# Performance work log

Hardware: AMD Instinct MI355X
Metric: run time of the kernel (lower is better)

The kernel has to match this reference:

```python
import jax, jax.numpy as jnp
import numpy as np

HEAD_DIM = 128
HIDDEN = 5120
NUM_KV_GROUPS = 8
NUM_MODALITIES = 3
NUM_Q_HEADS = 40
QKV_PER_MOD = NUM_Q_HEADS * HEAD_DIM + 2 * NUM_KV_GROUPS * HEAD_DIM + NUM_Q_HEADS  # 7208


def _rms_norm(x, w, eps=1e-6):
    xf = x.astype(jnp.float32)
    inv = jax.lax.rsqrt(jnp.mean(xf * xf, axis=-1, keepdims=True) + eps)
    return (xf * inv).astype(x.dtype) * w


def _apply_rope(x, cos, sin):
    # x: [B,S,H,D], cos/sin: [B,S,rd]
    rd = cos.shape[-1]
    xr, xp = x[..., :rd], x[..., rd:]
    c, s = cos[:, :, None, :], sin[:, :, None, :]
    x1, x2 = xr[..., : rd // 2], xr[..., rd // 2:]
    rot = jnp.concatenate([-x2, x1], axis=-1)
    return jnp.concatenate([xr * c + rot * s, xp], axis=-1)


def setup_inputs() -> dict:
    key = jax.random.key(0)
    ks = jax.random.split(key, 6)
    B, S = 1, 2048
    return {
        "x": jax.random.normal(ks[0], (B, S, HIDDEN), jnp.float32),
        "rope_cos": jax.random.uniform(ks[1], (B, S, HEAD_DIM), jnp.float32),
        "rope_sin": jax.random.uniform(ks[2], (B, S, HEAD_DIM), jnp.float32),
        "modality_ids": jax.random.randint(ks[3], (B, S), 0, NUM_MODALITIES, jnp.int32),
        "pre_norm": jnp.ones((NUM_MODALITIES * HIDDEN,), jnp.float32),
        "qkv_w": jax.random.normal(ks[4], (NUM_MODALITIES * QKV_PER_MOD, HIDDEN), jnp.float32) * 0.02,
        "q_norm": jnp.ones((NUM_MODALITIES * HEAD_DIM,), jnp.float32),
        "k_norm": jnp.ones((NUM_MODALITIES * HEAD_DIM,), jnp.float32),
        "proj_w": jax.random.normal(ks[5], (NUM_MODALITIES * HIDDEN, HIDDEN), jnp.float32) * 0.02,
    }


def reference(x, rope_cos, rope_sin, modality_ids, pre_norm, qkv_w, q_norm, k_norm, proj_w):
    B, S, _ = x.shape
    # per-token modality gather of pre-norm weight
    norm_w = pre_norm.reshape(NUM_MODALITIES, HIDDEN)[modality_ids]  # [B,S,H]
    normed = _rms_norm(x, norm_w)

    # modality-routed QKV: compute all modalities, select with one-hot (dense, jit-friendly)
    oh = jax.nn.one_hot(modality_ids, NUM_MODALITIES, dtype=x.dtype)  # [B,S,M]
    qkv_w3 = qkv_w.reshape(NUM_MODALITIES, QKV_PER_MOD, HIDDEN)
    qkv_all = jnp.einsum("bsh,moh->bsmo", normed, qkv_w3)  # [B,S,M,QKV]
    qkv = jnp.einsum("bsm,bsmo->bso", oh, qkv_all)

    q_dim = NUM_Q_HEADS * HEAD_DIM
    k_dim = NUM_KV_GROUPS * HEAD_DIM
    q = qkv[..., :q_dim].reshape(B, S, NUM_Q_HEADS, HEAD_DIM)
    k = qkv[..., q_dim:q_dim + k_dim].reshape(B, S, NUM_KV_GROUPS, HEAD_DIM)
    v = qkv[..., q_dim + k_dim:q_dim + 2 * k_dim].reshape(B, S, NUM_KV_GROUPS, HEAD_DIM)
    gate = jax.nn.sigmoid(qkv[..., q_dim + 2 * k_dim:q_dim + 2 * k_dim + NUM_Q_HEADS])  # [B,S,NQ]

    qn = q_norm.reshape(NUM_MODALITIES, HEAD_DIM)[modality_ids][:, :, None, :]  # [B,S,1,D]
    kn = k_norm.reshape(NUM_MODALITIES, HEAD_DIM)[modality_ids][:, :, None, :]
    q = _rms_norm(q, qn)
    k = _rms_norm(k, kn)

    q = _apply_rope(q, rope_cos, rope_sin)
    k = _apply_rope(k, rope_cos, rope_sin)

    repeat = NUM_Q_HEADS // NUM_KV_GROUPS
    k = jnp.repeat(k, repeat, axis=2)  # [B,S,NQ,D]
    v = jnp.repeat(v, repeat, axis=2)

    scale = 1.0 / np.sqrt(HEAD_DIM)
    scores = jnp.einsum("bqhd,bkhd->bhqk", q, k) * scale  # [B,NQ,S,S]
    attn = jax.nn.softmax(scores, axis=-1)
    out = jnp.einsum("bhqk,bkhd->bqhd", attn, v)  # [B,S,NQ,D]

    out = (out * gate[..., None]).reshape(B, S, NUM_Q_HEADS * HEAD_DIM)

    proj_w3 = proj_w.reshape(NUM_MODALITIES, HIDDEN, HIDDEN)
    proj_all = jnp.einsum("bsh,moh->bsmo", out, proj_w3)  # [B,S,M,H]
    return jnp.einsum("bsm,bsmo->bso", oh, proj_all)
```

## Files before the change

kernel.cpp:

```cpp
#include <hip/hip_runtime.h>

typedef _Float16 f16;
typedef f16 f16x8 __attribute__((ext_vector_type(8)));
typedef f16 f16x4 __attribute__((ext_vector_type(4)));
typedef float f32x4 __attribute__((ext_vector_type(4)));

#define HID 5120
#define QKVO 7208
#define S_TOK 2048
#define NQH 40
#define NKV 8
#define HD 128

__device__ __forceinline__ void gload16(const void* g, void* l) {
    __builtin_amdgcn_global_load_lds(
        (const __attribute__((address_space(1))) void*)g,
        (__attribute__((address_space(3))) void*)l,
        16, 0, 0);
}

__global__ void sort_tokens(const int* __restrict__ mod, int* __restrict__ sorted,
                            int* __restrict__ offs)
{
    int tid = threadIdx.x, wave = tid >> 6, lane = tid & 63;
    int mloc[8];
    int c[3] = {0, 0, 0};
#pragma unroll
    for (int j = 0; j < 8; ++j) {
        int m = mod[tid * 8 + j];
        mloc[j] = m;
        c[m]++;
    }
    __shared__ int wsum[4][3];
    int excl[3];
#pragma unroll
    for (int m = 0; m < 3; ++m) {
        int v = c[m];
        int incl = v;
        for (int d = 1; d < 64; d <<= 1) {
            int n = __shfl_up(incl, d, 64);
            if (lane >= d) incl += n;
        }
        excl[m] = incl - v;
        if (lane == 63) wsum[wave][m] = incl;
    }
    __syncthreads();
    int wbase[3], tot[3];
#pragma unroll
    for (int m = 0; m < 3; ++m) {
        int b = 0, t = 0;
        for (int w = 0; w < 4; ++w) {
            if (w < wave) b += wsum[w][m];
            t += wsum[w][m];
        }
        wbase[m] = b;
        tot[m] = t;
    }
    int base[3];
    base[0] = 0;
    base[1] = tot[0];
    base[2] = tot[0] + tot[1];
    if (tid == 0) {
        offs[0] = 0;
        offs[1] = tot[0];
        offs[2] = tot[0] + tot[1];
        offs[3] = S_TOK;
    }
    int pos[3];
#pragma unroll
    for (int m = 0; m < 3; ++m) pos[m] = base[m] + wbase[m] + excl[m];
#pragma unroll
    for (int j = 0; j < 8; ++j) {
        int m = mloc[j];
        sorted[pos[m]++] = tid * 8 + j;
    }
}

__global__ void cvt_f32_f16(const float* __restrict__ src, f16* __restrict__ dst, int n4)
{
    int i = blockIdx.x * 256 + threadIdx.x;
    int stride = gridDim.x * 256;
    const float4* s4 = (const float4*)src;
    f16x4* d4 = (f16x4*)dst;
    for (; i < n4; i += stride) {
        float4 a = s4[i];
        f16x4 h;
        h[0] = (f16)a.x; h[1] = (f16)a.y; h[2] = (f16)a.z; h[3] = (f16)a.w;
        d4[i] = h;
    }
}

__global__ void rms_pre(const float* __restrict__ x, const int* __restrict__ mod,
                        const float* __restrict__ prenorm, f16* __restrict__ A1)
{
    int tok = blockIdx.x, tid = threadIdx.x;
    int m = mod[tok];
    const float4* xv = (const float4*)(x + (size_t)tok * HID);
    float4 v[5];
    float ss = 0.f;
#pragma unroll
    for (int j = 0; j < 5; ++j) {
        v[j] = xv[tid + 256 * j];
        ss += v[j].x * v[j].x + v[j].y * v[j].y + v[j].z * v[j].z + v[j].w * v[j].w;
    }
    for (int d = 1; d < 64; d <<= 1) ss += __shfl_xor(ss, d, 64);
    __shared__ float ws[4];
    if ((tid & 63) == 0) ws[tid >> 6] = ss;
    __syncthreads();
    float tot = ws[0] + ws[1] + ws[2] + ws[3];
    float inv = rsqrtf(tot * (1.f / HID) + 1e-6f);
    const float4* wv = (const float4*)(prenorm + (size_t)m * HID);
    f16x4* out4 = (f16x4*)(A1 + (size_t)tok * HID);
#pragma unroll
    for (int j = 0; j < 5; ++j) {
        float4 w = wv[tid + 256 * j];
        f16x4 h;
        h[0] = (f16)(v[j].x * inv * w.x);
        h[1] = (f16)(v[j].y * inv * w.y);
        h[2] = (f16)(v[j].z * inv * w.z);
        h[3] = (f16)(v[j].w * inv * w.w);
        out4[tid + 256 * j] = h;
    }
}

__global__ void gemm_grouped(const f16* __restrict__ A, const f16* __restrict__ W,
                             float* __restrict__ C,
                             const int* __restrict__ sorted_tok,
                             const int* __restrict__ mod_off, int NW)
{
    const int K = HID;
    int nt = blockIdx.x, mt = blockIdx.y, mod = blockIdx.z;
    int off = mod_off[mod], cnt = mod_off[mod + 1] - off;
    if (mt * 128 >= cnt) return;
    __shared__ __align__(16) f16 As[128 * 64];
    __shared__ __align__(16) f16 Bs[128 * 64];
    __shared__ int rowtok[128];
    int tid = threadIdx.x, wave = tid >> 6, lane = tid & 63;
    if (tid < 128) {
        int r = mt * 128 + tid;
        rowtok[tid] = (r < cnt) ? sorted_tok[off + r] : -1;
    }
    __syncthreads();
    int wr = wave >> 1, wc = wave & 1;
    f32x4 acc[4][4] = {};
    const f16* Wm = W + (size_t)mod * NW * K;
    for (int kt = 0; kt < K / 64; ++kt) {
        int k0 = kt * 64;
#pragma unroll
        for (int it = 0; it < 4; ++it) {
            int c = it * 256 + tid;
            int row = c >> 3, kc = c & 7, skc = kc ^ (row & 7);
            int tk = rowtok[row];
            if (tk < 0) tk = 0;
            gload16(A + (size_t)tk * K + k0 + skc * 8, &As[c * 8]);
        }
#pragma unroll
        for (int it = 0; it < 4; ++it) {
            int c = it * 256 + tid;
            int row = c >> 3, kc = c & 7, skc = kc ^ (row & 7);
            int o = nt * 128 + row;
            if (o >= NW) o = NW - 1;
            gload16(Wm + (size_t)o * K + k0 + skc * 8, &Bs[c * 8]);
        }
        __syncthreads();
#pragma unroll
        for (int ks = 0; ks < 2; ++ks) {
            f16x8 a[4], b[4];
#pragma unroll
            for (int i = 0; i < 4; ++i) {
                int ar = wr * 64 + i * 16 + (lane & 15);
                int ac = (ks * 4 + (lane >> 4)) ^ (ar & 7);
                a[i] = *(const f16x8*)&As[ar * 64 + ac * 8];
                int br = wc * 64 + i * 16 + (lane & 15);
                int bc = (ks * 4 + (lane >> 4)) ^ (br & 7);
                b[i] = *(const f16x8*)&Bs[br * 64 + bc * 8];
            }
#pragma unroll
            for (int mi = 0; mi < 4; ++mi)
#pragma unroll
                for (int nj = 0; nj < 4; ++nj)
                    acc[mi][nj] = __builtin_amdgcn_mfma_f32_16x16x32_f16(
                        a[mi], b[nj], acc[mi][nj], 0, 0, 0);
        }
        __syncthreads();
    }
    int cl = lane & 15, rg = lane >> 4;
#pragma unroll
    for (int mi = 0; mi < 4; ++mi) {
#pragma unroll
        for (int rr = 0; rr < 4; ++rr) {
            int row = wr * 64 + mi * 16 + rg * 4 + rr;
            int tk = rowtok[row];
            if (tk < 0) continue;
            float* crow = C + (size_t)tk * NW;
#pragma unroll
            for (int nj = 0; nj < 4; ++nj) {
                int o = nt * 128 + wc * 64 + nj * 16 + cl;
                if (o < NW) crow[o] = acc[mi][nj][rr];
            }
        }
    }
}

__global__ void qkv_post(const float* __restrict__ qkv, const int* __restrict__ mod,
                         const float* __restrict__ cosb, const float* __restrict__ sinb,
                         const float* __restrict__ qnorm, const float* __restrict__ knorm,
                         f16* __restrict__ Qb, f16* __restrict__ Kb, float* __restrict__ gateb)
{
    int tok = blockIdx.x, tid = threadIdx.x;
    int wave = tid >> 6, lane = tid & 63;
    int m = mod[tok];
    float c0 = cosb[tok * HD + lane], c1 = cosb[tok * HD + 64 + lane];
    float s0 = sinb[tok * HD + lane], s1 = sinb[tok * HD + 64 + lane];
    const float* row = qkv + (size_t)tok * QKVO;
    for (int u = wave; u < 48; u += 4) {
        int base = (u < 40) ? u * HD : NQH * HD + (u - 40) * HD;
        float x0 = row[base + lane];
        float x1 = row[base + 64 + lane];
        float ss = x0 * x0 + x1 * x1;
        for (int d = 1; d < 64; d <<= 1) ss += __shfl_xor(ss, d, 64);
        float inv = rsqrtf(ss * (1.f / HD) + 1e-6f);
        const float* nw = (u < 40 ? qnorm : knorm) + m * HD;
        float n0 = x0 * inv * nw[lane];
        float n1 = x1 * inv * nw[64 + lane];
        float r0 = n0 * c0 - n1 * s0;
        float r1 = n1 * c1 + n0 * s1;
        if (u < 40) {
            const float sc = 0.08838834764831845f;
            r0 *= sc; r1 *= sc;
            Qb[((size_t)u * S_TOK + tok) * HD + lane] = (f16)r0;
            Qb[((size_t)u * S_TOK + tok) * HD + 64 + lane] = (f16)r1;
        } else {
            Kb[((size_t)(u - 40) * S_TOK + tok) * HD + lane] = (f16)r0;
            Kb[((size_t)(u - 40) * S_TOK + tok) * HD + 64 + lane] = (f16)r1;
        }
    }
    if (tid < 40) {
        float g = row[NQH * HD + 2 * NKV * HD + tid];
        gateb[tok * 40 + tid] = 1.f / (1.f + __expf(-g));
    }
}

__global__ void vtrans(const float* __restrict__ qkv, f16* __restrict__ Vt)
{
    int tc = blockIdx.x;
    int g = blockIdx.y;
    int tid = threadIdx.x;
    __shared__ float tile[64][129];
#pragma unroll
    for (int it = 0; it < 8; ++it) {
        int idx = it * 256 + tid;
        int r = idx >> 5, c4 = idx & 31;
        float4 v = *(const float4*)(qkv + (size_t)(tc * 64 + r) * QKVO + NQH * HD + NKV * HD + g * HD + c4 * 4);
        tile[r][c4 * 4 + 0] = v.x;
        tile[r][c4 * 4 + 1] = v.y;
        tile[r][c4 * 4 + 2] = v.z;
        tile[r][c4 * 4 + 3] = v.w;
    }
    __syncthreads();
    int d = tid >> 1, half = tid & 1;
    f16* dst = Vt + ((size_t)g * HD + d) * S_TOK + tc * 64 + half * 32;
#pragma unroll
    for (int j = 0; j < 32; ++j) dst[j] = (f16)tile[half * 32 + j][d];
}

__global__ void attn(const f16* __restrict__ Qb, const f16* __restrict__ Kb,
                     const f16* __restrict__ Vtb, const float* __restrict__ gateb,
                     f16* __restrict__ A2)
{
    int qt = blockIdx.x, h = blockIdx.y, grp = h / 5;
    int tid = threadIdx.x, wave = tid >> 6, lane = tid & 63;
    __shared__ __align__(16) f16 Qs[64 * 128];
    __shared__ __align__(16) f16 Ks[64 * 128];
    __shared__ __align__(16) f16 Vs[128 * 64];
    __shared__ __align__(16) f16 Ps[4][16 * 64];
    const f16* Qg = Qb + ((size_t)h * S_TOK + qt * 64) * HD;
#pragma unroll
    for (int it = 0; it < 4; ++it) {
        int c = it * 256 + tid, row = c >> 4, kc = c & 15, skc = kc ^ (row & 15);
        gload16(Qg + row * HD + skc * 8, &Qs[c * 8]);
    }
    __syncthreads();
    f16x8 qf[4];
    {
        int row = wave * 16 + (lane & 15);
#pragma unroll
        for (int ks = 0; ks < 4; ++ks) {
            int sk = (ks * 4 + (lane >> 4)) ^ (row & 15);
            qf[ks] = *(const f16x8*)&Qs[row * 128 + sk * 8];
        }
    }
    f32x4 o[8] = {};
    float mrow[4] = {-3.0e38f, -3.0e38f, -3.0e38f, -3.0e38f};
    float lrow[4] = {0.f, 0.f, 0.f, 0.f};
    const f16* Kg = Kb + (size_t)grp * S_TOK * HD;
    const f16* Vg = Vtb + (size_t)grp * HD * S_TOK;
    char* pbase = (char*)&Ps[wave][0];
    for (int t = 0; t < 32; ++t) {
#pragma unroll
        for (int it = 0; it < 4; ++it) {
            int c = it * 256 + tid, row = c >> 4, kc = c & 15, skc = kc ^ (row & 15);
            gload16(Kg + (size_t)(t * 64 + row) * HD + skc * 8, &Ks[c * 8]);
        }
#pragma unroll
        for (int it = 0; it < 4; ++it) {
            int c = it * 256 + tid, row = c >> 3, kc = c & 7, skc = kc ^ (row & 7);
            gload16(Vg + (size_t)row * S_TOK + t * 64 + skc * 8, &Vs[c * 8]);
        }
        __syncthreads();
        f32x4 s[4] = {};
#pragma unroll
        for (int ks = 0; ks < 4; ++ks) {
#pragma unroll
            for (int nj = 0; nj < 4; ++nj) {
                int kr = nj * 16 + (lane & 15);
                int sk = (ks * 4 + (lane >> 4)) ^ (kr & 15);
                f16x8 kf = *(const f16x8*)&Ks[kr * 128 + sk * 8];
                s[nj] = __builtin_amdgcn_mfma_f32_16x16x32_f16(qf[ks], kf, s[nj], 0, 0, 0);
            }
        }
        float mx[4], corr[4], psum[4];
#pragma unroll
        for (int r = 0; r < 4; ++r)
            mx[r] = fmaxf(fmaxf(s[0][r], s[1][r]), fmaxf(s[2][r], s[3][r]));
        for (int d = 1; d < 16; d <<= 1) {
#pragma unroll
            for (int r = 0; r < 4; ++r) mx[r] = fmaxf(mx[r], __shfl_xor(mx[r], d, 16));
        }
#pragma unroll
        for (int r = 0; r < 4; ++r) {
            float mn = fmaxf(mrow[r], mx[r]);
            corr[r] = __expf(mrow[r] - mn);
            mrow[r] = mn;
            psum[r] = 0.f;
        }
#pragma unroll
        for (int nj = 0; nj < 4; ++nj) {
#pragma unroll
            for (int r = 0; r < 4; ++r) {
                float p = __expf(s[nj][r] - mrow[r]);
                psum[r] += p;
                int prow = (lane >> 4) * 4 + r, col = (lane & 15) + nj * 16;
                int addr = (prow * 128 + col * 2) ^ ((prow & 7) << 4);
                *(f16*)(pbase + addr) = (f16)p;
            }
        }
        for (int d = 1; d < 16; d <<= 1) {
#pragma unroll
            for (int r = 0; r < 4; ++r) psum[r] += __shfl_xor(psum[r], d, 16);
        }
#pragma unroll
        for (int r = 0; r < 4; ++r) lrow[r] = lrow[r] * corr[r] + psum[r];
#pragma unroll
        for (int nj2 = 0; nj2 < 8; ++nj2)
#pragma unroll
            for (int r = 0; r < 4; ++r) o[nj2][r] *= corr[r];
#pragma unroll
        for (int ks2 = 0; ks2 < 2; ++ks2) {
            int prow = lane & 15;
            int sk = (ks2 * 4 + (lane >> 4)) ^ (prow & 7);
            f16x8 pa = *(const f16x8*)(pbase + prow * 128 + sk * 16);
#pragma unroll
            for (int nj2 = 0; nj2 < 8; ++nj2) {
                int vr = nj2 * 16 + (lane & 15);
                int skv = (ks2 * 4 + (lane >> 4)) ^ (vr & 7);
                f16x8 vf = *(const f16x8*)&Vs[vr * 64 + skv * 8];
                o[nj2] = __builtin_amdgcn_mfma_f32_16x16x32_f16(pa, vf, o[nj2], 0, 0, 0);
            }
        }
        __syncthreads();
    }
    int rbase = qt * 64 + wave * 16 + (lane >> 4) * 4;
#pragma unroll
    for (int r = 0; r < 4; ++r) {
        int tok = rbase + r;
        float sc = gateb[tok * 40 + h] / lrow[r];
#pragma unroll
        for (int nj2 = 0; nj2 < 8; ++nj2) {
            int d = nj2 * 16 + (lane & 15);
            A2[(size_t)tok * HID + h * HD + d] = (f16)(o[nj2][r] * sc);
        }
    }
}

extern "C" void kernel_launch(void* const* d_in, const int* in_sizes, int n_in,
                              void* d_out, int out_size, void* d_ws, size_t ws_size,
                              hipStream_t stream)
{
    const float* x = (const float*)d_in[0];
    const float* rc = (const float*)d_in[1];
    const float* rs = (const float*)d_in[2];
    const int* mod = (const int*)d_in[3];
    const float* prenorm = (const float*)d_in[4];
    const float* qkvw = (const float*)d_in[5];
    const float* qn = (const float*)d_in[6];
    const float* kn = (const float*)d_in[7];
    const float* projw = (const float*)d_in[8];
    float* out = (float*)d_out;

    char* p = (char*)d_ws;
    auto alloc = [&](size_t bytes) {
        char* r = p;
        p += (bytes + 255) & ~(size_t)255;
        return r;
    };
    int* sorted = (int*)alloc(S_TOK * 4);
    int* offs = (int*)alloc(16);
    f16* A1 = (f16*)alloc((size_t)S_TOK * HID * 2);
    f16* Wq = (f16*)alloc((size_t)3 * QKVO * HID * 2);
    f16* Wp = (f16*)alloc((size_t)3 * HID * HID * 2);
    float* qkv = (float*)alloc((size_t)S_TOK * QKVO * 4);
    f16* Qb = (f16*)alloc((size_t)NQH * S_TOK * HD * 2);
    f16* Kb = (f16*)alloc((size_t)NKV * S_TOK * HD * 2);
    f16* Vt = (f16*)alloc((size_t)NKV * HD * S_TOK * 2);
    float* gate = (float*)alloc((size_t)S_TOK * 40 * 4);
    f16* A2 = (f16*)alloc((size_t)S_TOK * HID * 2);
    if ((size_t)(p - (char*)d_ws) > ws_size) return;

    sort_tokens<<<1, 256, 0, stream>>>(mod, sorted, offs);
    cvt_f32_f16<<<2048, 256, 0, stream>>>(qkvw, Wq, 3 * QKVO * HID / 4);
    cvt_f32_f16<<<2048, 256, 0, stream>>>(projw, Wp, 3 * HID * HID / 4);
    rms_pre<<<2048, 256, 0, stream>>>(x, mod, prenorm, A1);
    gemm_grouped<<<dim3(57, 16, 3), 256, 0, stream>>>(A1, Wq, qkv, sorted, offs, QKVO);
    qkv_post<<<2048, 256, 0, stream>>>(qkv, mod, rc, rs, qn, kn, Qb, Kb, gate);
    vtrans<<<dim3(32, 8), 256, 0, stream>>>(qkv, Vt);
    attn<<<dim3(32, 40), 256, 0, stream>>>(Qb, Kb, Vt, gate, A2);
    gemm_grouped<<<dim3(40, 16, 3), 256, 0, stream>>>(A2, Wp, out, sorted, offs, HID);
}
```

Before: 939.7 us.

## Fuse fp32-to-fp16 weight conversion into grouped GEMM B-tile loads

Drops the two standalone conversion kernels that turned the QKV and projection weights into fp16 buffers. The grouped GEMM now reads fp32 weights directly, converts them in registers and stores them to LDS. The grid is reordered so the token-tile index varies fastest, letting blocks that share a weight tile run close together and reuse it from cache. The cost is that B loads become synchronous register loads instead of async global-to-LDS copies, and each fp32 weight tile may be fetched several times at double the byte size.

```diff
diff --git a/kernel.cpp b/kernel.cpp
--- a/kernel.cpp
+++ b/kernel.cpp
@@ -76,20 +76,6 @@
     }
 }
 
-__global__ void cvt_f32_f16(const float* __restrict__ src, f16* __restrict__ dst, int n4)
-{
-    int i = blockIdx.x * 256 + threadIdx.x;
-    int stride = gridDim.x * 256;
-    const float4* s4 = (const float4*)src;
-    f16x4* d4 = (f16x4*)dst;
-    for (; i < n4; i += stride) {
-        float4 a = s4[i];
-        f16x4 h;
-        h[0] = (f16)a.x; h[1] = (f16)a.y; h[2] = (f16)a.z; h[3] = (f16)a.w;
-        d4[i] = h;
-    }
-}
-
 __global__ void rms_pre(const float* __restrict__ x, const int* __restrict__ mod,
                         const float* __restrict__ prenorm, f16* __restrict__ A1)
 {
@@ -123,13 +109,13 @@
     }
 }
 
-__global__ void gemm_grouped(const f16* __restrict__ A, const f16* __restrict__ W,
+__global__ void gemm_grouped(const f16* __restrict__ A, const float* __restrict__ W,
                              float* __restrict__ C,
                              const int* __restrict__ sorted_tok,
                              const int* __restrict__ mod_off, int NW)
 {
     const int K = HID;
-    int nt = blockIdx.x, mt = blockIdx.y, mod = blockIdx.z;
+    int mt = blockIdx.x, nt = blockIdx.y, mod = blockIdx.z;
     int off = mod_off[mod], cnt = mod_off[mod + 1] - off;
     if (mt * 128 >= cnt) return;
     __shared__ __align__(16) f16 As[128 * 64];
@@ -143,7 +129,7 @@
     __syncthreads();
     int wr = wave >> 1, wc = wave & 1;
     f32x4 acc[4][4] = {};
-    const f16* Wm = W + (size_t)mod * NW * K;
+    const float* Wm = W + (size_t)mod * NW * K;
     for (int kt = 0; kt < K / 64; ++kt) {
         int k0 = kt * 64;
 #pragma unroll
@@ -160,7 +146,12 @@
             int row = c >> 3, kc = c & 7, skc = kc ^ (row & 7);
             int o = nt * 128 + row;
             if (o >= NW) o = NW - 1;
-            gload16(Wm + (size_t)o * K + k0 + skc * 8, &Bs[c * 8]);
+            const float4* src = (const float4*)(Wm + (size_t)o * K + k0 + skc * 8);
+            float4 lo = src[0], hi = src[1];
+            f16x8 h;
+            h[0] = (f16)lo.x; h[1] = (f16)lo.y; h[2] = (f16)lo.z; h[3] = (f16)lo.w;
+            h[4] = (f16)hi.x; h[5] = (f16)hi.y; h[6] = (f16)hi.z; h[7] = (f16)hi.w;
+            *(f16x8*)&Bs[c * 8] = h;
         }
         __syncthreads();
 #pragma unroll
@@ -407,8 +398,6 @@
     int* sorted = (int*)alloc(S_TOK * 4);
     int* offs = (int*)alloc(16);
     f16* A1 = (f16*)alloc((size_t)S_TOK * HID * 2);
-    f16* Wq = (f16*)alloc((size_t)3 * QKVO * HID * 2);
-    f16* Wp = (f16*)alloc((size_t)3 * HID * HID * 2);
     float* qkv = (float*)alloc((size_t)S_TOK * QKVO * 4);
     f16* Qb = (f16*)alloc((size_t)NQH * S_TOK * HD * 2);
     f16* Kb = (f16*)alloc((size_t)NKV * S_TOK * HD * 2);
@@ -418,12 +407,10 @@
     if ((size_t)(p - (char*)d_ws) > ws_size) return;
 
     sort_tokens<<<1, 256, 0, stream>>>(mod, sorted, offs);
-    cvt_f32_f16<<<2048, 256, 0, stream>>>(qkvw, Wq, 3 * QKVO * HID / 4);
-    cvt_f32_f16<<<2048, 256, 0, stream>>>(projw, Wp, 3 * HID * HID / 4);
     rms_pre<<<2048, 256, 0, stream>>>(x, mod, prenorm, A1);
-    gemm_grouped<<<dim3(57, 16, 3), 256, 0, stream>>>(A1, Wq, qkv, sorted, offs, QKVO);
+    gemm_grouped<<<dim3(16, 57, 3), 256, 0, stream>>>(A1, qkvw, qkv, sorted, offs, QKVO);
     qkv_post<<<2048, 256, 0, stream>>>(qkv, mod, rc, rs, qn, kn, Qb, Kb, gate);
     vtrans<<<dim3(32, 8), 256, 0, stream>>>(qkv, Vt);
     attn<<<dim3(32, 40), 256, 0, stream>>>(Qb, Kb, Vt, gate, A2);
-    gemm_grouped<<<dim3(40, 16, 3), 256, 0, stream>>>(A2, Wp, out, sorted, offs, HID);
-}
+    gemm_grouped<<<dim3(16, 40, 3), 256, 0, stream>>>(A2, projw, out, sorted, offs, HID);
+}
```

Result: slower. 1.613 ms (+71.6%).
